# Performance work log

Measured on AMD Instinct MI355X. Metric: run time of the kernel, lower is better.

The kernel has to match this reference:

```python
import jax, jax.numpy as jnp
import numpy as np

D_MODEL = 1024
D_FF = 2048
NUM_EXPERTS = 16
TOP_K = 2
CAPACITY_FACTOR = 1.25
BATCH, SEQ = 4, 2048


def setup_inputs() -> dict:
    key = jax.random.key(0)
    k0, k1, k2, k3 = jax.random.split(key, 4)
    x = jax.random.normal(k0, (BATCH, SEQ, D_MODEL), jnp.float32)
    gate_w = jax.random.normal(k1, (NUM_EXPERTS, D_MODEL), jnp.float32) / np.float32(np.sqrt(D_MODEL))
    w1 = jax.random.normal(k2, (NUM_EXPERTS, D_MODEL, D_FF), jnp.float32) / np.float32(np.sqrt(D_MODEL))
    w2 = jax.random.normal(k3, (NUM_EXPERTS, D_FF, D_MODEL), jnp.float32) / np.float32(np.sqrt(D_FF))
    return {"x": x, "gate_w": gate_w, "w1": w1, "w2": w2}


def reference(x, gate_w, w1, w2):
    B, S, d = x.shape
    T = B * S
    E, K = NUM_EXPERTS, TOP_K
    capacity = int(CAPACITY_FACTOR * T * K / E)  # static

    xf = x.reshape(T, d)                                  # [T, d]
    logits = xf @ gate_w.T                                # [T, E]
    probs = jax.nn.sigmoid(logits)
    top_vals, sel = jax.lax.top_k(probs, K)               # [T, K]
    weights = top_vals / (top_vals.sum(-1, keepdims=True) + 1e-6)

    # Capacity-based ranking: rank of each (token, slot) within its expert,
    # in flattened token-major order (matches torch cumsum over one-hot).
    flat_sel = sel.reshape(-1)                            # [T*K]
    onehot = jax.nn.one_hot(flat_sel, E, dtype=jnp.int32)
    ranks = jnp.take_along_axis(jnp.cumsum(onehot, axis=0), flat_sel[:, None], axis=1)[:, 0] - 1
    valid = ranks < capacity                              # [T*K]

    sentinel = E * capacity
    slot = jnp.where(valid, flat_sel * capacity + ranks, sentinel)

    # token-major repeat matches x_flat.unsqueeze(1).expand(-1,K,-1).reshape(-1,d)
    x_rep = jnp.repeat(xf, K, axis=0)                     # [T*K, d]
    padded = jnp.zeros((sentinel + 1, d), xf.dtype).at[slot].set(x_rep)
    padded = padded[:sentinel].reshape(E, capacity, d)    # [E, C, d]

    h = jax.nn.gelu(jnp.einsum('ecd,edf->ecf', padded, w1), approximate=False)
    out_padded = jnp.einsum('ecf,efd->ecd', h, w2).reshape(sentinel, d)

    gathered = out_padded[jnp.minimum(slot, sentinel - 1)]
    gathered = jnp.where(valid[:, None], gathered, jnp.zeros((), xf.dtype))
    out = (gathered * weights.reshape(-1)[:, None]).reshape(T, K, d).sum(axis=1)
    return out.reshape(B, S, d)
```

## Files before the change

kernel.cpp:

```cpp
#include <hip/hip_runtime.h>
#include <math.h>

#define T_TOK 8192
#define DM 1024
#define DF 2048
#define NE 16
#define TK 2
#define CAP 1280

typedef __bf16 bf16x8 __attribute__((ext_vector_type(8)));
typedef float f32x4 __attribute__((ext_vector_type(4)));

__device__ __forceinline__ unsigned short f2bf(float f) {
  unsigned int u = __float_as_uint(f);
  unsigned int r = (u + 0x7fffu + ((u >> 16) & 1u)) >> 16;
  return (unsigned short)r;
}

__device__ __forceinline__ float bf2f(unsigned short u) {
  return __uint_as_float((unsigned int)u << 16);
}

__device__ __forceinline__ void async_copy16(const void* g, void* l) {
  __builtin_amdgcn_global_load_lds(
      (const __attribute__((address_space(1))) void*)g,
      (__attribute__((address_space(3))) void*)l, 16, 0, 0);
}

__global__ __launch_bounds__(256) void transpose_conv_kernel(
    const float* __restrict__ in, unsigned short* __restrict__ out, int R, int Cc) {
  __shared__ unsigned short tl[64][72];
  size_t eoff = (size_t)blockIdx.z * R * Cc;
  in += eoff; out += eoff;
  int c0 = blockIdx.x * 64, r0 = blockIdx.y * 64;
  int t = threadIdx.x;
#pragma unroll
  for (int i = 0; i < 4; i++) {
    int r = (t >> 4) + i * 16;
    int c = (t & 15) * 4;
    float4 v = *(const float4*)(in + (size_t)(r0 + r) * Cc + c0 + c);
    tl[c + 0][r] = f2bf(v.x);
    tl[c + 1][r] = f2bf(v.y);
    tl[c + 2][r] = f2bf(v.z);
    tl[c + 3][r] = f2bf(v.w);
  }
  __syncthreads();
#pragma unroll
  for (int i = 0; i < 2; i++) {
    int c = (t >> 3) + i * 32;
    int r = (t & 7) * 8;
    *(int4*)(out + (size_t)(c0 + c) * R + r0 + r) = *(const int4*)&tl[c][r];
  }
}

__global__ __launch_bounds__(256) void gate_kernel(
    const float* __restrict__ x, const float* __restrict__ gw,
    int* __restrict__ sel, float* __restrict__ wts) {
  __shared__ float sgw[NE * DM];
  int tid = threadIdx.x, lane = tid & 63, wv = tid >> 6;
  for (int i = tid; i < NE * DM / 4; i += 256)
    ((float4*)sgw)[i] = ((const float4*)gw)[i];
  __syncthreads();
  const float4* g4 = (const float4*)sgw;
  for (int it = 0; it < 16; it++) {
    int t = blockIdx.x * 64 + wv * 16 + it;
    const float4* xr = (const float4*)(x + (size_t)t * DM);
    float4 xv[4];
#pragma unroll
    for (int j = 0; j < 4; j++) xv[j] = xr[j * 64 + lane];
    float acc[NE];
#pragma unroll
    for (int e = 0; e < NE; e++) {
      float s = 0.f;
#pragma unroll
      for (int j = 0; j < 4; j++) {
        float4 g = g4[e * 256 + j * 64 + lane];
        s += xv[j].x * g.x + xv[j].y * g.y + xv[j].z * g.z + xv[j].w * g.w;
      }
      acc[e] = s;
    }
#pragma unroll
    for (int e = 0; e < NE; e++) {
      float v = acc[e];
#pragma unroll
      for (int off = 32; off > 0; off >>= 1) v += __shfl_xor(v, off);
      acc[e] = v;
    }
    if (lane == 0) {
      float p[NE];
#pragma unroll
      for (int e = 0; e < NE; e++) p[e] = 1.f / (1.f + expf(-acc[e]));
      int i0 = 0;
#pragma unroll
      for (int e = 1; e < NE; e++) if (p[e] > p[i0]) i0 = e;
      int i1 = (i0 == 0) ? 1 : 0;
#pragma unroll
      for (int e = 0; e < NE; e++) if (e != i0 && p[e] > p[i1]) i1 = e;
      float v0 = p[i0], v1 = p[i1], s = v0 + v1 + 1e-6f;
      sel[2 * t] = i0; sel[2 * t + 1] = i1;
      wts[2 * t] = v0 / s; wts[2 * t + 1] = v1 / s;
    }
  }
}

__global__ __launch_bounds__(1024) void scan_kernel(
    const int* __restrict__ sel, int* __restrict__ pos_slot,
    int* __restrict__ exp_tok, int* __restrict__ counts) {
  int e = blockIdx.x;
  int tid = threadIdx.x, lane = tid & 63, wv = tid >> 6;
  __shared__ int wtot[16];
  int local[16];
  unsigned int flags = 0;
  int run = 0;
#pragma unroll
  for (int it = 0; it < 16; it++) {
    int p = wv * 1024 + it * 64 + lane;
    int f = (sel[p] == e) ? 1 : 0;
    unsigned long long b = __ballot(f);
    if (f) { flags |= 1u << it; local[it] = run + __popcll(b & ((1ull << lane) - 1ull)); }
    run += __popcll(b);
  }
  if (lane == 0) wtot[wv] = run;
  __syncthreads();
  int base = 0, total = 0;
#pragma unroll
  for (int i = 0; i < 16; i++) {
    int v = wtot[i];
    if (i < wv) base += v;
    total += v;
  }
#pragma unroll
  for (int it = 0; it < 16; it++) {
    if (flags & (1u << it)) {
      int p = wv * 1024 + it * 64 + lane;
      int rank = base + local[it];
      if (rank < CAP) {
        pos_slot[p] = e * CAP + rank;
        exp_tok[e * CAP + rank] = p;
      } else {
        pos_slot[p] = -1;
      }
    }
  }
  if (tid == 0) counts[e] = total < CAP ? total : CAP;
}

__global__ __launch_bounds__(128) void gather_kernel(
    const float* __restrict__ x, const int* __restrict__ exp_tok,
    const int* __restrict__ counts, unsigned short* __restrict__ Xp) {
  int i = blockIdx.x, e = blockIdx.y;
  int tid = threadIdx.x;
  unsigned short* dst = Xp + ((size_t)e * CAP + i) * DM;
  int4 pk = make_int4(0, 0, 0, 0);
  if (i < counts[e]) {
    int p = exp_tok[e * CAP + i];
    int t = p >> 1;
    const float4* src = (const float4*)(x + (size_t)t * DM);
    float4 v0 = src[tid * 2];
    float4 v1 = src[tid * 2 + 1];
    union { unsigned short u[8]; int4 v; } q;
    q.u[0] = f2bf(v0.x); q.u[1] = f2bf(v0.y); q.u[2] = f2bf(v0.z); q.u[3] = f2bf(v0.w);
    q.u[4] = f2bf(v1.x); q.u[5] = f2bf(v1.y); q.u[6] = f2bf(v1.z); q.u[7] = f2bf(v1.w);
    pk = q.v;
  }
  ((int4*)dst)[tid] = pk;
}

template <bool GELU>
__global__ __launch_bounds__(256) void gemm_kernel(
    const unsigned short* __restrict__ A, const unsigned short* __restrict__ Bt,
    unsigned short* __restrict__ C, const int* __restrict__ counts,
    int N, int K, size_t sA, size_t sB, size_t sC) {
  int e = blockIdx.z;
  int m0 = blockIdx.y * 128;
  int cnt = counts[e];
  if (m0 >= cnt) return;
  __shared__ unsigned short As[128 * 32];
  __shared__ unsigned short Bs[128 * 32];
  A += (size_t)e * sA;
  Bt += (size_t)e * sB;
  C += (size_t)e * sC;
  int n0 = blockIdx.x * 128;
  int tid = threadIdx.x;
  int lane = tid & 63;
  int wv = tid >> 6;
  int wm = (wv >> 1) * 64, wn = (wv & 1) * 64;
  int qd = lane >> 4, lm = lane & 15;
  int sa = (lm >> 1) & 3;
  int chunk = (tid & 3) ^ ((tid >> 3) & 3);

  const unsigned short* a0 = A + (size_t)(m0 + (tid >> 2)) * K + chunk * 8;
  const unsigned short* a1 = a0 + (size_t)64 * K;
  const unsigned short* b0 = Bt + (size_t)(n0 + (tid >> 2)) * K + chunk * 8;
  const unsigned short* b1 = b0 + (size_t)64 * K;
  char* lAs = (char*)As;
  char* lBs = (char*)Bs;

  f32x4 acc[4][4] = {};
  for (int k0 = 0; k0 < K; k0 += 32) {
    __syncthreads();
    async_copy16(a0 + k0, lAs + tid * 16);
    async_copy16(a1 + k0, lAs + (tid + 256) * 16);
    async_copy16(b0 + k0, lBs + tid * 16);
    async_copy16(b1 + k0, lBs + (tid + 256) * 16);
    __syncthreads();
    bf16x8 af[4], bfr[4];
#pragma unroll
    for (int i = 0; i < 4; i++)
      af[i] = *(const bf16x8*)(lAs + (wm + i * 16 + lm) * 64 + (qd ^ sa) * 16);
#pragma unroll
    for (int j = 0; j < 4; j++)
      bfr[j] = *(const bf16x8*)(lBs + (wn + j * 16 + lm) * 64 + (qd ^ sa) * 16);
#pragma unroll
    for (int i = 0; i < 4; i++)
#pragma unroll
      for (int j = 0; j < 4; j++)
        acc[i][j] = __builtin_amdgcn_mfma_f32_16x16x32_bf16(af[i], bfr[j], acc[i][j], 0, 0, 0);
  }
#pragma unroll
  for (int i = 0; i < 4; i++) {
    int row = m0 + wm + i * 16 + qd * 4;
#pragma unroll
    for (int j = 0; j < 4; j++) {
      int col = n0 + wn + j * 16 + lm;
#pragma unroll
      for (int r = 0; r < 4; r++) {
        float v = acc[i][j][r];
        if (GELU) v = 0.5f * v * (1.f + erff(v * 0.70710678118f));
        C[(size_t)(row + r) * N + col] = f2bf(v);
      }
    }
  }
}

__global__ __launch_bounds__(128) void combine_kernel(
    const unsigned short* __restrict__ outp, const int* __restrict__ pos_slot,
    const float* __restrict__ wts, float* __restrict__ out) {
  int t = blockIdx.x, tid = threadIdx.x;
  float acc[8] = {0.f, 0.f, 0.f, 0.f, 0.f, 0.f, 0.f, 0.f};
#pragma unroll
  for (int k = 0; k < 2; k++) {
    int p = 2 * t + k;
    int s = pos_slot[p];
    if (s >= 0) {
      float w = wts[p];
      union { int4 v; unsigned short u[8]; } q;
      q.v = *(const int4*)(outp + (size_t)s * DM + tid * 8);
#pragma unroll
      for (int i = 0; i < 8; i++) acc[i] += w * bf2f(q.u[i]);
    }
  }
  float4* dst = (float4*)(out + (size_t)t * DM + tid * 8);
  dst[0] = make_float4(acc[0], acc[1], acc[2], acc[3]);
  dst[1] = make_float4(acc[4], acc[5], acc[6], acc[7]);
}

extern "C" void kernel_launch(void* const* d_in, const int* in_sizes, int n_in,
                              void* d_out, int out_size, void* d_ws, size_t ws_size,
                              hipStream_t stream) {
  (void)in_sizes; (void)n_in; (void)out_size; (void)ws_size;
  const float* x  = (const float*)d_in[0];
  const float* gw = (const float*)d_in[1];
  const float* w1 = (const float*)d_in[2];
  const float* w2 = (const float*)d_in[3];
  float* out = (float*)d_out;

  char* ws = (char*)d_ws;
  unsigned short* w1t = (unsigned short*)ws; ws += (size_t)NE * DM * DF * 2;
  unsigned short* w2t = (unsigned short*)ws; ws += (size_t)NE * DF * DM * 2;
  unsigned short* Xp  = (unsigned short*)ws; ws += (size_t)NE * CAP * DM * 2;
  unsigned short* H   = (unsigned short*)ws; ws += (size_t)NE * CAP * DF * 2;
  unsigned short* outp = (unsigned short*)ws; ws += (size_t)NE * CAP * DM * 2;
  int* sel = (int*)ws;       ws += (size_t)T_TOK * TK * 4;
  float* wts = (float*)ws;   ws += (size_t)T_TOK * TK * 4;
  int* pos_slot = (int*)ws;  ws += (size_t)T_TOK * TK * 4;
  int* exp_tok = (int*)ws;   ws += (size_t)NE * CAP * 4;
  int* counts = (int*)ws;    ws += (size_t)NE * 4;

  transpose_conv_kernel<<<dim3(DF / 64, DM / 64, NE), 256, 0, stream>>>(w1, w1t, DM, DF);
  transpose_conv_kernel<<<dim3(DM / 64, DF / 64, NE), 256, 0, stream>>>(w2, w2t, DF, DM);
  gate_kernel<<<T_TOK / 64, 256, 0, stream>>>(x, gw, sel, wts);
  scan_kernel<<<NE, 1024, 0, stream>>>(sel, pos_slot, exp_tok, counts);
  gather_kernel<<<dim3(CAP, NE), 128, 0, stream>>>(x, exp_tok, counts, Xp);
  gemm_kernel<true><<<dim3(DF / 128, CAP / 128, NE), 256, 0, stream>>>(
      Xp, w1t, H, counts, DF, DM, (size_t)CAP * DM, (size_t)DM * DF, (size_t)CAP * DF);
  gemm_kernel<false><<<dim3(DM / 128, CAP / 128, NE), 256, 0, stream>>>(
      H, w2t, outp, counts, DM, DF, (size_t)CAP * DF, (size_t)DF * DM, (size_t)CAP * DM);
  combine_kernel<<<T_TOK, 128, 0, stream>>>(outp, pos_slot, wts, out);
}
```

Measured before the change: 763.5 us.

## Merge gate and weight transposes into one prep kernel; swap GEMM operand roles

The two weight transpose/convert launches and the gate kernel are combined into a single prep kernel that dispatches on block index, with the gate now computing one token per wave and reading gate weights from global memory instead of shared memory. The GEMMs swap operands so the weights act as the M operand and tokens as N. This lets the epilogue write four contiguous bf16 values per store rather than scattered scalar stores. The prep merge cuts launch count and lets gating overlap with the transposes, at the cost of gate-weight reads no longer being staged in LDS.

```diff
diff --git a/kernel.cpp b/kernel.cpp
--- a/kernel.cpp
+++ b/kernel.cpp
@@ -10,6 +10,7 @@
 
 typedef __bf16 bf16x8 __attribute__((ext_vector_type(8)));
 typedef float f32x4 __attribute__((ext_vector_type(4)));
+typedef unsigned short us4 __attribute__((ext_vector_type(4)));
 
 __device__ __forceinline__ unsigned short f2bf(float f) {
   unsigned int u = __float_as_uint(f);
@@ -27,47 +28,23 @@
       (__attribute__((address_space(3))) void*)l, 16, 0, 0);
 }
 
-__global__ __launch_bounds__(256) void transpose_conv_kernel(
-    const float* __restrict__ in, unsigned short* __restrict__ out, int R, int Cc) {
+#define GATE_BLKS (T_TOK / 4)
+__global__ __launch_bounds__(256) void prep_kernel(
+    const float* __restrict__ x, const float* __restrict__ gw,
+    const float* __restrict__ w1, const float* __restrict__ w2,
+    unsigned short* __restrict__ w1t, unsigned short* __restrict__ w2t,
+    int* __restrict__ sel, float* __restrict__ wts) {
   __shared__ unsigned short tl[64][72];
-  size_t eoff = (size_t)blockIdx.z * R * Cc;
-  in += eoff; out += eoff;
-  int c0 = blockIdx.x * 64, r0 = blockIdx.y * 64;
-  int t = threadIdx.x;
-#pragma unroll
-  for (int i = 0; i < 4; i++) {
-    int r = (t >> 4) + i * 16;
-    int c = (t & 15) * 4;
-    float4 v = *(const float4*)(in + (size_t)(r0 + r) * Cc + c0 + c);
-    tl[c + 0][r] = f2bf(v.x);
-    tl[c + 1][r] = f2bf(v.y);
-    tl[c + 2][r] = f2bf(v.z);
-    tl[c + 3][r] = f2bf(v.w);
-  }
-  __syncthreads();
-#pragma unroll
-  for (int i = 0; i < 2; i++) {
-    int c = (t >> 3) + i * 32;
-    int r = (t & 7) * 8;
-    *(int4*)(out + (size_t)(c0 + c) * R + r0 + r) = *(const int4*)&tl[c][r];
-  }
-}
-
-__global__ __launch_bounds__(256) void gate_kernel(
-    const float* __restrict__ x, const float* __restrict__ gw,
-    int* __restrict__ sel, float* __restrict__ wts) {
-  __shared__ float sgw[NE * DM];
-  int tid = threadIdx.x, lane = tid & 63, wv = tid >> 6;
-  for (int i = tid; i < NE * DM / 4; i += 256)
-    ((float4*)sgw)[i] = ((const float4*)gw)[i];
-  __syncthreads();
-  const float4* g4 = (const float4*)sgw;
-  for (int it = 0; it < 16; it++) {
-    int t = blockIdx.x * 64 + wv * 16 + it;
+  int b = blockIdx.x;
+  int tid = threadIdx.x;
+  if (b < GATE_BLKS) {
+    int lane = tid & 63, wv = tid >> 6;
+    int t = b * 4 + wv;
     const float4* xr = (const float4*)(x + (size_t)t * DM);
     float4 xv[4];
 #pragma unroll
     for (int j = 0; j < 4; j++) xv[j] = xr[j * 64 + lane];
+    const float4* g4 = (const float4*)gw;
     float acc[NE];
 #pragma unroll
     for (int e = 0; e < NE; e++) {
@@ -99,6 +76,37 @@
       float v0 = p[i0], v1 = p[i1], s = v0 + v1 + 1e-6f;
       sel[2 * t] = i0; sel[2 * t + 1] = i1;
       wts[2 * t] = v0 / s; wts[2 * t + 1] = v1 / s;
+    }
+  } else {
+    int bb = b - GATE_BLKS;
+    const float* in; unsigned short* out; int R, Cc, rt, ct, e;
+    if (bb < 8192) {
+      in = w1; out = w1t; R = DM; Cc = DF;
+      e = bb >> 9; int r = bb & 511; rt = r >> 5; ct = r & 31;
+    } else {
+      bb -= 8192;
+      in = w2; out = w2t; R = DF; Cc = DM;
+      e = bb >> 9; int r = bb & 511; rt = r >> 4; ct = r & 15;
+    }
+    size_t eoff = (size_t)e * R * Cc;
+    in += eoff; out += eoff;
+    int c0 = ct * 64, r0 = rt * 64;
+#pragma unroll
+    for (int i = 0; i < 4; i++) {
+      int r = (tid >> 4) + i * 16;
+      int c = (tid & 15) * 4;
+      float4 v = *(const float4*)(in + (size_t)(r0 + r) * Cc + c0 + c);
+      tl[c + 0][r] = f2bf(v.x);
+      tl[c + 1][r] = f2bf(v.y);
+      tl[c + 2][r] = f2bf(v.z);
+      tl[c + 3][r] = f2bf(v.w);
+    }
+    __syncthreads();
+#pragma unroll
+    for (int i = 0; i < 2; i++) {
+      int c = (tid >> 3) + i * 32;
+      int r = (tid & 7) * 8;
+      *(int4*)(out + (size_t)(c0 + c) * R + r0 + r) = *(const int4*)&tl[c][r];
     }
   }
 }
@@ -170,17 +178,17 @@
 __global__ __launch_bounds__(256) void gemm_kernel(
     const unsigned short* __restrict__ A, const unsigned short* __restrict__ Bt,
     unsigned short* __restrict__ C, const int* __restrict__ counts,
-    int N, int K, size_t sA, size_t sB, size_t sC) {
+    int M, int K, size_t sA, size_t sB, size_t sC) {
   int e = blockIdx.z;
-  int m0 = blockIdx.y * 128;
+  int n0 = blockIdx.x * 128;
   int cnt = counts[e];
-  if (m0 >= cnt) return;
+  if (n0 >= cnt) return;
   __shared__ unsigned short As[128 * 32];
   __shared__ unsigned short Bs[128 * 32];
   A += (size_t)e * sA;
   Bt += (size_t)e * sB;
   C += (size_t)e * sC;
-  int n0 = blockIdx.x * 128;
+  int m0 = blockIdx.y * 128;
   int tid = threadIdx.x;
   int lane = tid & 63;
   int wv = tid >> 6;
@@ -218,17 +226,20 @@
         acc[i][j] = __builtin_amdgcn_mfma_f32_16x16x32_bf16(af[i], bfr[j], acc[i][j], 0, 0, 0);
   }
 #pragma unroll
-  for (int i = 0; i < 4; i++) {
-    int row = m0 + wm + i * 16 + qd * 4;
-#pragma unroll
-    for (int j = 0; j < 4; j++) {
-      int col = n0 + wn + j * 16 + lm;
+  for (int j = 0; j < 4; j++) {
+    int slot = n0 + wn + j * 16 + lm;
+    unsigned short* crow = C + (size_t)slot * M;
+#pragma unroll
+    for (int i = 0; i < 4; i++) {
+      int m = m0 + wm + i * 16 + qd * 4;
+      us4 pk;
 #pragma unroll
       for (int r = 0; r < 4; r++) {
         float v = acc[i][j][r];
         if (GELU) v = 0.5f * v * (1.f + erff(v * 0.70710678118f));
-        C[(size_t)(row + r) * N + col] = f2bf(v);
+        pk[r] = f2bf(v);
       }
+      *(us4*)(crow + m) = pk;
     }
   }
 }
@@ -277,14 +288,12 @@
   int* exp_tok = (int*)ws;   ws += (size_t)NE * CAP * 4;
   int* counts = (int*)ws;    ws += (size_t)NE * 4;
 
-  transpose_conv_kernel<<<dim3(DF / 64, DM / 64, NE), 256, 0, stream>>>(w1, w1t, DM, DF);
-  transpose_conv_kernel<<<dim3(DM / 64, DF / 64, NE), 256, 0, stream>>>(w2, w2t, DF, DM);
-  gate_kernel<<<T_TOK / 64, 256, 0, stream>>>(x, gw, sel, wts);
+  prep_kernel<<<GATE_BLKS + 16384, 256, 0, stream>>>(x, gw, w1, w2, w1t, w2t, sel, wts);
   scan_kernel<<<NE, 1024, 0, stream>>>(sel, pos_slot, exp_tok, counts);
   gather_kernel<<<dim3(CAP, NE), 128, 0, stream>>>(x, exp_tok, counts, Xp);
-  gemm_kernel<true><<<dim3(DF / 128, CAP / 128, NE), 256, 0, stream>>>(
-      Xp, w1t, H, counts, DF, DM, (size_t)CAP * DM, (size_t)DM * DF, (size_t)CAP * DF);
-  gemm_kernel<false><<<dim3(DM / 128, CAP / 128, NE), 256, 0, stream>>>(
-      H, w2t, outp, counts, DM, DF, (size_t)CAP * DF, (size_t)DF * DM, (size_t)CAP * DM);
+  gemm_kernel<true><<<dim3(CAP / 128, DF / 128, NE), 256, 0, stream>>>(
+      w1t, Xp, H, counts, DF, DM, (size_t)DM * DF, (size_t)CAP * DM, (size_t)CAP * DF);
+  gemm_kernel<false><<<dim3(CAP / 128, DM / 128, NE), 256, 0, stream>>>(
+      w2t, H, outp, counts, DM, DF, (size_t)DF * DM, (size_t)CAP * DF, (size_t)CAP * DM);
   combine_kernel<<<T_TOK, 128, 0, stream>>>(outp, pos_slot, wts, out);
 }
```

Measured after the change: 660.6 us. 1.16x faster.
